# Kernel optimization log

Hardware: AMD Instinct MI355X
Metric: run time of the kernel (lower is better)

Reference implementation:

```python
import jax, jax.numpy as jnp
import numpy as np

D_MODEL = 1024
D = 512
B = 32
L = 1024


def setup_inputs() -> dict:
    key = jax.random.key(0)
    ks = jax.random.split(key, 8)
    s = 1.0 / np.sqrt(D_MODEL)
    x = jax.random.normal(ks[0], (B, L, D_MODEL), dtype=jnp.float32)
    mask = jnp.ones((B, 1, L), dtype=jnp.int32)  # padding mask; 1 = keep
    Wq = jax.random.uniform(ks[1], (D, D_MODEL), jnp.float32, -s, s)
    bq = jax.random.uniform(ks[2], (D,), jnp.float32, -s, s)
    Wk = jax.random.uniform(ks[3], (D, D_MODEL), jnp.float32, -s, s)
    bk = jax.random.uniform(ks[4], (D,), jnp.float32, -s, s)
    Wv = jax.random.uniform(ks[5], (D, D_MODEL), jnp.float32, -s, s)
    bv = jax.random.uniform(ks[6], (D,), jnp.float32, -s, s)
    return {"x": x, "Wq": Wq, "bq": bq, "Wk": Wk, "bk": bk, "Wv": Wv, "bv": bv, "mask": mask}


def reference(x, Wq, bq, Wk, bk, Wv, bv, mask):
    Bq, Lq, _ = x.shape
    q = jnp.einsum('blc,dc->bld', x, Wq) + bq  # [B,L,D]
    k = jnp.einsum('blc,dc->bld', x, Wk) + bk
    v = jnp.einsum('blc,dc->bld', x, Wv) + bv
    scale = k.shape[-1] ** -0.5
    weights = jnp.einsum('bid,bjd->bij', q, k) * scale  # [B,L,L]
    causal = jnp.tril(jnp.ones((Lq, Lq), dtype=bool))
    neg_inf = jnp.float32(-jnp.inf)
    weights = jnp.where(causal[None, :, :], weights, neg_inf)
    weights = jnp.where(mask == 0, neg_inf, weights)  # mask broadcasts [B,1,L]
    weights = jax.nn.softmax(weights, axis=-1)
    # NOTE: source calls self.dropout(weights) but discards result -> no-op
    out = jnp.einsum('bij,bjd->bid', weights, v)
    return jax.nn.relu(out)
```

## Files before the change

### kernel.cpp

```cpp
#include <hip/hip_runtime.h>
#include <hip/hip_bf16.h>
#include <stdint.h>

#define DM 1024
#define DD 512
#define BB 32
#define LL 1024
#define SCALE 0.04419417382415922f
#define MAT ((size_t)BB * LL * DD)

typedef float f32x4 __attribute__((ext_vector_type(4)));
typedef short bf16x8 __attribute__((ext_vector_type(8)));
typedef short bf16x4 __attribute__((ext_vector_type(4)));

__device__ inline unsigned short f2bf(float f) {
    union { float f; uint32_t u; } v; v.f = f;
    uint32_t r = v.u + 0x7fffu + ((v.u >> 16) & 1u);
    return (unsigned short)(r >> 16);
}

__device__ inline bf16x4 cvt4(f32x4 a, float s) {
    bf16x4 r;
    r[0] = (short)f2bf(a[0] * s);
    r[1] = (short)f2bf(a[1] * s);
    r[2] = (short)f2bf(a[2] * s);
    r[3] = (short)f2bf(a[3] * s);
    return r;
}

#define GLOAD_LDS16(gsrc, ldst) \
    __builtin_amdgcn_global_load_lds((const __attribute__((address_space(1))) unsigned int*)(gsrc), \
        (__attribute__((address_space(3))) unsigned int*)(ldst), 16, 0, 0)

__device__ inline void tile_barrier() {
    asm volatile("s_waitcnt vmcnt(0)" ::: "memory");
    __builtin_amdgcn_sched_barrier(0);
    __builtin_amdgcn_s_barrier();
    __builtin_amdgcn_sched_barrier(0);
}

__device__ inline void gate6() {
    asm volatile("s_waitcnt vmcnt(6)" ::: "memory");
    __builtin_amdgcn_sched_barrier(0);
    __builtin_amdgcn_s_barrier();
    __builtin_amdgcn_sched_barrier(0);
}
__device__ inline void gate4() {
    asm volatile("s_waitcnt vmcnt(4)" ::: "memory");
    __builtin_amdgcn_sched_barrier(0);
    __builtin_amdgcn_s_barrier();
    __builtin_amdgcn_sched_barrier(0);
}
__device__ inline void gate2() {
    asm volatile("s_waitcnt vmcnt(2)" ::: "memory");
    __builtin_amdgcn_sched_barrier(0);
    __builtin_amdgcn_s_barrier();
    __builtin_amdgcn_sched_barrier(0);
}
__device__ inline void gate0() {
    asm volatile("s_waitcnt vmcnt(0)" ::: "memory");
    __builtin_amdgcn_sched_barrier(0);
    __builtin_amdgcn_s_barrier();
    __builtin_amdgcn_sched_barrier(0);
}
__device__ inline void gateB() {
    __builtin_amdgcn_sched_barrier(0);
    __builtin_amdgcn_s_barrier();
    __builtin_amdgcn_sched_barrier(0);
}

__global__ __launch_bounds__(256) void cast_x(const float* __restrict__ x,
                                              unsigned short* __restrict__ xb)
{
    size_t idx = (size_t)blockIdx.x * 256 + threadIdx.x;
    size_t base = idx * 8;
    f32x4 a = *(const f32x4*)(x + base);
    f32x4 b = *(const f32x4*)(x + base + 4);
    bf16x4 lo = cvt4(a, 1.0f), hi = cvt4(b, 1.0f);
    bf16x8 o = {lo[0], lo[1], lo[2], lo[3], hi[0], hi[1], hi[2], hi[3]};
    *(bf16x8*)(xb + base) = o;
}

__global__ __launch_bounds__(256) void cast_w(const float* __restrict__ Wq,
                                              const float* __restrict__ Wk,
                                              const float* __restrict__ Wv,
                                              unsigned short* __restrict__ Wb)
{
    size_t idx = (size_t)blockIdx.x * 256 + threadIdx.x;
    int o = (int)(idx >> 16);
    size_t rem = idx & 65535;
    const float* W = (o == 0) ? Wq : (o == 1) ? Wk : Wv;
    float s = (o == 0) ? SCALE : 1.0f;
    size_t base = rem * 8;
    f32x4 a = *(const f32x4*)(W + base);
    f32x4 b = *(const f32x4*)(W + base + 4);
    bf16x4 lo = cvt4(a, s), hi = cvt4(b, s);
    bf16x8 out = {lo[0], lo[1], lo[2], lo[3], hi[0], hi[1], hi[2], hi[3]};
    *(bf16x8*)(Wb + (size_t)o * 524288 + base) = out;
}

__global__ __launch_bounds__(512, 2) void qkv_proj4(
    const unsigned short* __restrict__ xb,
    const unsigned short* __restrict__ Wb,
    const float* __restrict__ bq, const float* __restrict__ bk, const float* __restrict__ bv,
    unsigned short* __restrict__ qkv)
{
    __shared__ __align__(16) unsigned short AL[2][2][8192];
    __shared__ __align__(16) unsigned short BL[2][2][8192];

    const int o = blockIdx.y;
    const float* bias = (o == 0) ? bq : (o == 1) ? bk : bv;
    const float wscale = (o == 0) ? SCALE : 1.0f;
    const unsigned short* W = Wb + (size_t)o * 524288;
    unsigned short* out = qkv + (size_t)o * MAT;

    int wg = blockIdx.x;
    wg = (wg & 7) * 32 + (wg >> 3);
    const int mt = wg >> 1, nt = wg & 1;
    const int rowbase = mt * 256;
    const int colbase = nt * 256;

    const int tid  = threadIdx.x;
    const int lane = tid & 63;
    const int w    = tid >> 6;
    const int wm   = w >> 2;
    const int wn   = w & 3;
    const int l15  = lane & 15, l4 = lane >> 4;
    const int rxor = l15 & 7;

    const int r8   = lane >> 3;
    const int swch = (lane & 7) ^ r8;

    const char* xpanel = (const char*)(xb + (size_t)rowbase * DM);
    const char* wpanel = (const char*)(W  + (size_t)colbase * DM);

    #define STAGE_HALF(panel, T, H, slot) do {                                   \
        _Pragma("unroll")                                                        \
        for (int i2 = 0; i2 < 2; ++i2) {                                         \
            int grp = i2 * 8 + w;                                                \
            GLOAD_LDS16((panel) + ((size_t)((H) * 128 + grp * 8 + r8) * 2048)    \
                            + (size_t)(T) * 128 + swch * 16,                     \
                        (char*)(slot) + grp * 1024);                             \
        }                                                                        \
    } while (0)

    #define RDA(base, mf4, ks) (*(const bf16x8*)((base) + (wm * 64 + (mf4) * 16 + l15) * 128 \
                            + ((((ks) * 4 + l4) ^ rxor) << 4)))
    #define RDB(base, nfl, ks) (*(const bf16x8*)((base) + (wn * 32 + (nfl) * 16 + l15) * 128 \
                            + ((((ks) * 4 + l4) ^ rxor) << 4)))

    f32x4 acc[8][4];
    #pragma unroll
    for (int i = 0; i < 8; ++i)
        #pragma unroll
        for (int j = 0; j < 4; ++j)
            acc[i][j] = (f32x4){0.f, 0.f, 0.f, 0.f};

    bf16x8 aF[4][2], bF[4][2];

    STAGE_HALF(xpanel, 0, 0, &AL[0][0][0]);
    STAGE_HALF(wpanel, 0, 0, &BL[0][0][0]);
    STAGE_HALF(wpanel, 0, 1, &BL[0][1][0]);
    STAGE_HALF(xpanel, 0, 1, &AL[0][1][0]);

    for (int t = 0; t < 16; ++t) {
        const int c = t & 1, cn = c ^ 1;
        const char* A0b = (const char*)&AL[c][0][0];
        const char* A1b = (const char*)&AL[c][1][0];
        const char* B0b = (const char*)&BL[c][0][0];
        const char* B1b = (const char*)&BL[c][1][0];
        const bool st = (t < 15);

        if (st) { STAGE_HALF(xpanel, t + 1, 0, &AL[cn][0][0]); gate6(); } else gate4();
        #pragma unroll
        for (int ks = 0; ks < 2; ++ks) {
            #pragma unroll
            for (int mf = 0; mf < 4; ++mf) aF[mf][ks] = RDA(A0b, mf, ks);
            bF[0][ks] = RDB(B0b, 0, ks);
            bF[1][ks] = RDB(B0b, 1, ks);
        }
        #pragma unroll
        for (int ks = 0; ks < 2; ++ks)
            #pragma unroll
            for (int nf = 0; nf < 2; ++nf)
                #pragma unroll
                for (int mf = 0; mf < 4; ++mf)
                    acc[mf][nf] = __builtin_amdgcn_mfma_f32_16x16x32_bf16(aF[mf][ks], bF[nf][ks], acc[mf][nf], 0, 0, 0);

        if (st) { STAGE_HALF(wpanel, t + 1, 0, &BL[cn][0][0]); gate6(); } else gate2();
        #pragma unroll
        for (int ks = 0; ks < 2; ++ks) {
            bF[2][ks] = RDB(B1b, 0, ks);
            bF[3][ks] = RDB(B1b, 1, ks);
        }
        #pragma unroll
        for (int ks = 0; ks < 2; ++ks)
            #pragma unroll
            for (int nf = 0; nf < 2; ++nf)
                #pragma unroll
                for (int mf = 0; mf < 4; ++mf)
                    acc[mf][2 + nf] = __builtin_amdgcn_mfma_f32_16x16x32_bf16(aF[mf][ks], bF[2 + nf][ks], acc[mf][2 + nf], 0, 0, 0);

        if (st) { STAGE_HALF(wpanel, t + 1, 1, &BL[cn][1][0]); gate6(); } else gate0();
        #pragma unroll
        for (int ks = 0; ks < 2; ++ks)
            #pragma unroll
            for (int mf = 0; mf < 4; ++mf) aF[mf][ks] = RDA(A1b, mf, ks);
        #pragma unroll
        for (int ks = 0; ks < 2; ++ks)
            #pragma unroll
            for (int nf = 0; nf < 2; ++nf)
                #pragma unroll
                for (int mf = 0; mf < 4; ++mf)
                    acc[4 + mf][nf] = __builtin_amdgcn_mfma_f32_16x16x32_bf16(aF[mf][ks], bF[nf][ks], acc[4 + mf][nf], 0, 0, 0);

        if (st) STAGE_HALF(xpanel, t + 1, 1, &AL[cn][1][0]);
        gateB();
        #pragma unroll
        for (int ks = 0; ks < 2; ++ks)
            #pragma unroll
            for (int nf = 0; nf < 2; ++nf)
                #pragma unroll
                for (int mf = 0; mf < 4; ++mf)
                    acc[4 + mf][2 + nf] = __builtin_amdgcn_mfma_f32_16x16x32_bf16(aF[mf][ks], bF[2 + nf][ks], acc[4 + mf][2 + nf], 0, 0, 0);
    }
    #undef STAGE_HALF
    #undef RDA
    #undef RDB

    #pragma unroll
    for (int nf = 0; nf < 4; ++nf) {
        int col = colbase + ((nf < 2) ? wn * 32 + nf * 16 : 128 + wn * 32 + (nf - 2) * 16) + l15;
        float bv_ = bias[col] * wscale;
        #pragma unroll
        for (int mf = 0; mf < 8; ++mf) {
            int row0 = rowbase + ((mf < 4) ? wm * 64 + mf * 16 : 128 + wm * 64 + (mf - 4) * 16) + l4 * 4;
            #pragma unroll
            for (int r = 0; r < 4; ++r)
                out[(size_t)(row0 + r) * DD + col] = f2bf(acc[mf][nf][r] + bv_);
        }
    }
}

__global__ __launch_bounds__(256) void vtrans(const unsigned short* __restrict__ v,
                                              unsigned short* __restrict__ vt)
{
    __shared__ unsigned short T[64][72];
    const int lt = blockIdx.x, dt = blockIdx.y, b = blockIdx.z;
    const int t = threadIdx.x;
    const unsigned short* src = v + ((size_t)(b * LL + lt * 64)) * DD + dt * 64;
    #pragma unroll
    for (int it = 0; it < 2; ++it) {
        int r  = (t >> 3) + it * 32;
        int c0 = (t & 7) * 8;
        bf16x8 x = *(const bf16x8*)(src + (size_t)r * DD + c0);
        *(bf16x4*)&T[r][c0]     = (bf16x4){x[0], x[1], x[2], x[3]};
        *(bf16x4*)&T[r][c0 + 4] = (bf16x4){x[4], x[5], x[6], x[7]};
    }
    __syncthreads();
    unsigned short* dst = vt + ((size_t)(b * DD + dt * 64)) * LL + lt * 64;
    #pragma unroll
    for (int it = 0; it < 2; ++it) {
        int d  = (t >> 3) + it * 32;
        int c0 = (t & 7) * 8;
        bf16x8 o;
        #pragma unroll
        for (int e = 0; e < 8; ++e) o[e] = T[c0 + e][d];
        *(bf16x8*)(dst + (size_t)d * LL + c0) = o;
    }
}

__global__ __launch_bounds__(256, 1) void attn3(
    const unsigned short* __restrict__ qkv,
    const unsigned short* __restrict__ vt,
    const int* __restrict__ mask,
    float* __restrict__ outp)
{
    __shared__ __align__(16) unsigned short KtL[2][16384];
    __shared__ __align__(16) unsigned short VtL[2][16384];
    __shared__ __align__(16) unsigned short Pw[4][16][36];
    __shared__ float mbias[1024];

    const int bx = blockIdx.x;
    const int h = bx >> 8, i = bx & 255;
    const int b = i & 31;
    const int qtx = (i >> 5) & 7;
    const int qt = h ? qtx : 15 - qtx;

    const int tid = threadIdx.x, lane = tid & 63, w = tid >> 6;
    const int l15 = lane & 15, l4 = lane >> 4;
    const int lsw = lane * 16;

    const unsigned short* q = qkv;
    const unsigned short* k = qkv + MAT;
    const char* kb  = (const char*)k + ((size_t)b * LL) * DD * 2;
    const char* vtb = (const char*)vt + ((size_t)b * DD) * LL * 2;

    {
        const int* mp = mask + b * LL;
        #pragma unroll
        for (int j = 0; j < 4; ++j)
            mbias[tid * 4 + j] = mp[tid * 4 + j] ? 0.0f : -1e30f;
    }

    bf16x8 qf[16];
    {
        const unsigned short* qp = q + ((size_t)(b * LL + qt * 64 + w * 16 + l15)) * DD + l4 * 8;
        #pragma unroll
        for (int ks = 0; ks < 16; ++ks)
            qf[ks] = *(const bf16x8*)(qp + ks * 32);
    }

    f32x4 oacc[32];
    #pragma unroll
    for (int n = 0; n < 32; ++n) oacc[n] = (f32x4){0.f, 0.f, 0.f, 0.f};
    float mrow[4] = {-1e30f, -1e30f, -1e30f, -1e30f};
    float lrow[4] = {0.f, 0.f, 0.f, 0.f};

    const int jtmax = 2 * qt + 1;

    #define STAGE_KV(JT, BUF) do {                                              \
        const char* kt = kb + ((size_t)(JT) << 15);                             \
        char* ldsK = (char*)&KtL[(BUF)][0];                                     \
        _Pragma("unroll")                                                       \
        for (int i2 = 0; i2 < 8; ++i2) {                                        \
            int row = i2 * 4 + w;                                               \
            GLOAD_LDS16(kt + (row << 10) + (lsw ^ ((row & 7) << 4)),            \
                        ldsK + (row << 10));                                    \
        }                                                                       \
        const char* vtj = vtb + ((size_t)(JT) << 6);                            \
        char* ldsV = (char*)&VtL[(BUF)][0];                                     \
        _Pragma("unroll")                                                       \
        for (int i2 = 0; i2 < 8; ++i2) {                                        \
            int c0 = i2 * 256 + w * 64;                                         \
            int c  = c0 + lane;                                                 \
            GLOAD_LDS16(vtj + ((size_t)(c >> 2) << 11) + ((c & 3) << 4),        \
                        ldsV + c0 * 16);                                        \
        }                                                                       \
    } while (0)

    STAGE_KV(0, 0);
    __syncthreads();

    const int swz = (l15 & 7) << 4;

    for (int jt = 0; jt <= jtmax; ++jt) {
        const int cur = jt & 1;
        if (jt < jtmax) STAGE_KV(jt + 1, cur ^ 1);

        const char* Kc = (const char*)&KtL[cur][0];
        f32x4 sacc[2];
        sacc[0] = (f32x4){0.f, 0.f, 0.f, 0.f};
        sacc[1] = (f32x4){0.f, 0.f, 0.f, 0.f};
        #pragma unroll
        for (int ks = 0; ks < 16; ++ks) {
            int coloff = ((ks << 6) + (l4 << 4)) ^ swz;
            #pragma unroll
            for (int nf = 0; nf < 2; ++nf) {
                const bf16x8 kf = *(const bf16x8*)(Kc + ((nf * 16 + l15) << 10) + coloff);
                sacc[nf] = __builtin_amdgcn_mfma_f32_16x16x32_bf16(qf[ks], kf, sacc[nf], 0, 0, 0);
            }
        }

        const bool diag = (jt >= 2 * qt);
        float s[2][4];
        #pragma unroll
        for (int nf = 0; nf < 2; ++nf) {
            float bb_ = mbias[jt * 32 + nf * 16 + l15];
            #pragma unroll
            for (int r = 0; r < 4; ++r) {
                float val = sacc[nf][r] + bb_;
                if (diag) {
                    int gi = qt * 64 + w * 16 + l4 * 4 + r;
                    int gj = jt * 32 + nf * 16 + l15;
                    val = (gj <= gi) ? val : -3e38f;
                }
                s[nf][r] = val;
            }
        }
        float pm[4];
        #pragma unroll
        for (int r = 0; r < 4; ++r) {
            float mx = fmaxf(s[0][r], s[1][r]);
            mx = fmaxf(mx, __shfl_xor(mx, 1));
            mx = fmaxf(mx, __shfl_xor(mx, 2));
            mx = fmaxf(mx, __shfl_xor(mx, 4));
            mx = fmaxf(mx, __shfl_xor(mx, 8));
            pm[r] = mx;
        }
        bool need = false;
        #pragma unroll
        for (int r = 0; r < 4; ++r) need |= (pm[r] - mrow[r] > 8.0f);
        if (__any(need)) {
            #pragma unroll
            for (int r = 0; r < 4; ++r) {
                float mn = fmaxf(mrow[r], pm[r]);
                float corr = __expf(mrow[r] - mn);
                mrow[r] = mn;
                lrow[r] *= corr;
                #pragma unroll
                for (int n = 0; n < 32; ++n) oacc[n][r] *= corr;
            }
        }
        #pragma unroll
        for (int r = 0; r < 4; ++r) {
            float ls = 0.f;
            #pragma unroll
            for (int nf = 0; nf < 2; ++nf) {
                float p = __expf(s[nf][r] - mrow[r]);
                ls += p;
                Pw[w][l4 * 4 + r][nf * 16 + l15] = f2bf(p);
            }
            ls += __shfl_xor(ls, 1);
            ls += __shfl_xor(ls, 2);
            ls += __shfl_xor(ls, 4);
            ls += __shfl_xor(ls, 8);
            lrow[r] += ls;
        }

        const bf16x8 pa = *(const bf16x8*)&Pw[w][l15][l4 * 8];
        const char* Vc = (const char*)&VtL[cur][0];
        #pragma unroll
        for (int n = 0; n < 32; ++n) {
            const bf16x8 vb_ = *(const bf16x8*)(Vc + ((n * 16 + l15) << 6) + (l4 << 4));
            oacc[n] = __builtin_amdgcn_mfma_f32_16x16x32_bf16(pa, vb_, oacc[n], 0, 0, 0);
        }

        if (jt < jtmax) tile_barrier();
    }

    float inv[4];
    #pragma unroll
    for (int r = 0; r < 4; ++r) inv[r] = 1.0f / lrow[r];
    float* op = outp + ((size_t)(b * LL + qt * 64 + w * 16 + l4 * 4)) * DD + l15;
    #pragma unroll
    for (int n = 0; n < 32; ++n)
        #pragma unroll
        for (int r = 0; r < 4; ++r)
            op[(size_t)r * DD + n * 16] = fmaxf(oacc[n][r] * inv[r], 0.f);
    #undef STAGE_KV
}

extern "C" void kernel_launch(void* const* d_in, const int* in_sizes, int n_in,
                              void* d_out, int out_size, void* d_ws, size_t ws_size,
                              hipStream_t stream) {
    const float* x  = (const float*)d_in[0];
    const float* Wq = (const float*)d_in[1];
    const float* bq = (const float*)d_in[2];
    const float* Wk = (const float*)d_in[3];
    const float* bk = (const float*)d_in[4];
    const float* Wv = (const float*)d_in[5];
    const float* bv = (const float*)d_in[6];
    const int* mask = (const int*)d_in[7];

    unsigned short* qkv = (unsigned short*)d_ws;
    unsigned short* v   = qkv + 2 * MAT;
    unsigned short* vtp = qkv + 3 * MAT;
    unsigned short* Wb  = vtp;
    unsigned short* xb  = (unsigned short*)d_out;
    float* out = (float*)d_out;

    cast_x<<<16384, 256, 0, stream>>>(x, xb);
    cast_w<<<768, 256, 0, stream>>>(Wq, Wk, Wv, Wb);
    qkv_proj4<<<dim3(256, 3), 512, 0, stream>>>(xb, Wb, bq, bk, bv, qkv);
    vtrans<<<dim3(16, 8, 32), 256, 0, stream>>>(v, vtp);
    attn3<<<dim3(512), 256, 0, stream>>>(qkv, vtp, mask, out);
}
```

Before: 278.6 us.

## Single-buffer K/V LDS tiles with split staging and read mask from global

```diff
diff --git a/kernel.cpp b/kernel.cpp
--- a/kernel.cpp
+++ b/kernel.cpp
@@ -32,7 +32,7 @@
     __builtin_amdgcn_global_load_lds((const __attribute__((address_space(1))) unsigned int*)(gsrc), \
         (__attribute__((address_space(3))) unsigned int*)(ldst), 16, 0, 0)
 
-__device__ inline void tile_barrier() {
+__device__ inline void publish_barrier() {
     asm volatile("s_waitcnt vmcnt(0)" ::: "memory");
     __builtin_amdgcn_sched_barrier(0);
     __builtin_amdgcn_s_barrier();
@@ -64,6 +64,12 @@
     __builtin_amdgcn_sched_barrier(0);
 }
 __device__ inline void gateB() {
+    __builtin_amdgcn_sched_barrier(0);
+    __builtin_amdgcn_s_barrier();
+    __builtin_amdgcn_sched_barrier(0);
+}
+__device__ inline void gate8() {
+    asm volatile("s_waitcnt vmcnt(8)" ::: "memory");
     __builtin_amdgcn_sched_barrier(0);
     __builtin_amdgcn_s_barrier();
     __builtin_amdgcn_sched_barrier(0);
@@ -270,22 +276,19 @@
     }
 }
 
-__global__ __launch_bounds__(256, 1) void attn3(
+__global__ __launch_bounds__(256) void attn6(
     const unsigned short* __restrict__ qkv,
     const unsigned short* __restrict__ vt,
     const int* __restrict__ mask,
     float* __restrict__ outp)
 {
-    __shared__ __align__(16) unsigned short KtL[2][16384];
-    __shared__ __align__(16) unsigned short VtL[2][16384];
+    __shared__ __align__(16) unsigned short KtL[16384];
+    __shared__ __align__(16) unsigned short VtL[16384];
     __shared__ __align__(16) unsigned short Pw[4][16][36];
-    __shared__ float mbias[1024];
 
     const int bx = blockIdx.x;
-    const int h = bx >> 8, i = bx & 255;
-    const int b = i & 31;
-    const int qtx = (i >> 5) & 7;
-    const int qt = h ? qtx : 15 - qtx;
+    const int qt = (bx >> 4) & 15;
+    const int b  = (bx & 15) | ((bx >> 8) << 4);
 
     const int tid = threadIdx.x, lane = tid & 63, w = tid >> 6;
     const int l15 = lane & 15, l4 = lane >> 4;
@@ -295,13 +298,7 @@
     const unsigned short* k = qkv + MAT;
     const char* kb  = (const char*)k + ((size_t)b * LL) * DD * 2;
     const char* vtb = (const char*)vt + ((size_t)b * DD) * LL * 2;
-
-    {
-        const int* mp = mask + b * LL;
-        #pragma unroll
-        for (int j = 0; j < 4; ++j)
-            mbias[tid * 4 + j] = mp[tid * 4 + j] ? 0.0f : -1e30f;
-    }
+    const int* mp = mask + b * LL;
 
     bf16x8 qf[16];
     {
@@ -319,36 +316,35 @@
 
     const int jtmax = 2 * qt + 1;
 
-    #define STAGE_KV(JT, BUF) do {                                              \
+    #define STAGE_K6(JT) do {                                                   \
         const char* kt = kb + ((size_t)(JT) << 15);                             \
-        char* ldsK = (char*)&KtL[(BUF)][0];                                     \
         _Pragma("unroll")                                                       \
         for (int i2 = 0; i2 < 8; ++i2) {                                        \
             int row = i2 * 4 + w;                                               \
             GLOAD_LDS16(kt + (row << 10) + (lsw ^ ((row & 7) << 4)),            \
-                        ldsK + (row << 10));                                    \
+                        (char*)KtL + (row << 10));                              \
         }                                                                       \
+    } while (0)
+
+    #define STAGE_V6(JT) do {                                                   \
         const char* vtj = vtb + ((size_t)(JT) << 6);                            \
-        char* ldsV = (char*)&VtL[(BUF)][0];                                     \
         _Pragma("unroll")                                                       \
         for (int i2 = 0; i2 < 8; ++i2) {                                        \
             int c0 = i2 * 256 + w * 64;                                         \
             int c  = c0 + lane;                                                 \
             GLOAD_LDS16(vtj + ((size_t)(c >> 2) << 11) + ((c & 3) << 4),        \
-                        ldsV + c0 * 16);                                        \
+                        (char*)VtL + c0 * 16);                                  \
         }                                                                       \
     } while (0)
 
-    STAGE_KV(0, 0);
-    __syncthreads();
+    STAGE_K6(0);
+    STAGE_V6(0);
 
     const int swz = (l15 & 7) << 4;
 
     for (int jt = 0; jt <= jtmax; ++jt) {
-        const int cur = jt & 1;
-        if (jt < jtmax) STAGE_KV(jt + 1, cur ^ 1);
-
-        const char* Kc = (const char*)&KtL[cur][0];
+        gate8();
+
         f32x4 sacc[2];
         sacc[0] = (f32x4){0.f, 0.f, 0.f, 0.f};
         sacc[1] = (f32x4){0.f, 0.f, 0.f, 0.f};
@@ -357,16 +353,23 @@
             int coloff = ((ks << 6) + (l4 << 4)) ^ swz;
             #pragma unroll
             for (int nf = 0; nf < 2; ++nf) {
-                const bf16x8 kf = *(const bf16x8*)(Kc + ((nf * 16 + l15) << 10) + coloff);
+                const bf16x8 kf = *(const bf16x8*)((const char*)KtL + ((nf * 16 + l15) << 10) + coloff);
                 sacc[nf] = __builtin_amdgcn_mfma_f32_16x16x32_bf16(qf[ks], kf, sacc[nf], 0, 0, 0);
             }
         }
 
+        __builtin_amdgcn_sched_barrier(0);
+        __syncthreads();
+        __builtin_amdgcn_sched_barrier(0);
+        if (jt < jtmax) STAGE_K6(jt + 1);
+
         const bool diag = (jt >= 2 * qt);
+        float mb0 = mp[jt * 32 + l15]      ? 0.0f : -1e30f;
+        float mb1 = mp[jt * 32 + 16 + l15] ? 0.0f : -1e30f;
         float s[2][4];
         #pragma unroll
         for (int nf = 0; nf < 2; ++nf) {
-            float bb_ = mbias[jt * 32 + nf * 16 + l15];
+            float bb_ = nf ? mb1 : mb0;
             #pragma unroll
             for (int r = 0; r < 4; ++r) {
                 float val = sacc[nf][r] + bb_;
@@ -419,14 +422,16 @@
         }
 
         const bf16x8 pa = *(const bf16x8*)&Pw[w][l15][l4 * 8];
-        const char* Vc = (const char*)&VtL[cur][0];
         #pragma unroll
         for (int n = 0; n < 32; ++n) {
-            const bf16x8 vb_ = *(const bf16x8*)(Vc + ((n * 16 + l15) << 6) + (l4 << 4));
+            const bf16x8 vb_ = *(const bf16x8*)((const char*)VtL + ((n * 16 + l15) << 6) + (l4 << 4));
             oacc[n] = __builtin_amdgcn_mfma_f32_16x16x32_bf16(pa, vb_, oacc[n], 0, 0, 0);
         }
 
-        if (jt < jtmax) tile_barrier();
+        if (jt < jtmax) {
+            gateB();
+            STAGE_V6(jt + 1);
+        }
     }
 
     float inv[4];
@@ -438,7 +443,8 @@
         #pragma unroll
         for (int r = 0; r < 4; ++r)
             op[(size_t)r * DD + n * 16] = fmaxf(oacc[n][r] * inv[r], 0.f);
-    #undef STAGE_KV
+    #undef STAGE_K6
+    #undef STAGE_V6
 }
 
 extern "C" void kernel_launch(void* const* d_in, const int* in_sizes, int n_in,
@@ -464,5 +470,5 @@
     cast_w<<<768, 256, 0, stream>>>(Wq, Wk, Wv, Wb);
     qkv_proj4<<<dim3(256, 3), 512, 0, stream>>>(xb, Wb, bq, bk, bv, qkv);
     vtrans<<<dim3(16, 8, 32), 256, 0, stream>>>(v, vtp);
-    attn3<<<dim3(512), 256, 0, stream>>>(qkv, vtp, mask, out);
-}
+    attn6<<<dim3(512), 256, 0, stream>>>(qkv, vtp, mask, out);
+}
```

Result: slower. 335.9 us (+20.6%).

## Split fused flash attention into QK GEMM, row softmax and PV GEMM kernels

Applied to the files above, without the earlier changes.

```diff
diff --git a/kernel.cpp b/kernel.cpp
--- a/kernel.cpp
+++ b/kernel.cpp
@@ -17,6 +17,10 @@
     union { float f; uint32_t u; } v; v.f = f;
     uint32_t r = v.u + 0x7fffu + ((v.u >> 16) & 1u);
     return (unsigned short)(r >> 16);
+}
+__device__ inline float bf2f(unsigned short u) {
+    union { uint32_t u; float f; } v; v.u = ((uint32_t)u) << 16;
+    return v.f;
 }
 
 __device__ inline bf16x4 cvt4(f32x4 a, float s) {
@@ -32,13 +36,12 @@
     __builtin_amdgcn_global_load_lds((const __attribute__((address_space(1))) unsigned int*)(gsrc), \
         (__attribute__((address_space(3))) unsigned int*)(ldst), 16, 0, 0)
 
-__device__ inline void tile_barrier() {
+__device__ inline void publish_barrier() {
     asm volatile("s_waitcnt vmcnt(0)" ::: "memory");
     __builtin_amdgcn_sched_barrier(0);
     __builtin_amdgcn_s_barrier();
     __builtin_amdgcn_sched_barrier(0);
 }
-
 __device__ inline void gate6() {
     asm volatile("s_waitcnt vmcnt(6)" ::: "memory");
     __builtin_amdgcn_sched_barrier(0);
@@ -270,31 +273,105 @@
     }
 }
 
-__global__ __launch_bounds__(256, 1) void attn3(
+__global__ __launch_bounds__(256, 2) void sgemm_qk(
     const unsigned short* __restrict__ qkv,
-    const unsigned short* __restrict__ vt,
-    const int* __restrict__ mask,
-    float* __restrict__ outp)
-{
-    __shared__ __align__(16) unsigned short KtL[2][16384];
-    __shared__ __align__(16) unsigned short VtL[2][16384];
-    __shared__ __align__(16) unsigned short Pw[4][16][36];
-    __shared__ float mbias[1024];
-
-    const int bx = blockIdx.x;
-    const int h = bx >> 8, i = bx & 255;
-    const int b = i & 31;
-    const int qtx = (i >> 5) & 7;
-    const int qt = h ? qtx : 15 - qtx;
-
-    const int tid = threadIdx.x, lane = tid & 63, w = tid >> 6;
-    const int l15 = lane & 15, l4 = lane >> 4;
-    const int lsw = lane * 16;
+    unsigned short* __restrict__ S)
+{
+    __shared__ __align__(16) unsigned short At[2][8192];
+    __shared__ __align__(16) unsigned short Bt[2][8192];
+
+    int wg = blockIdx.x;
+    wg = (wg & 7) * 144 + (wg >> 3);
+    const int b = wg / 36;
+    const int t36 = wg % 36;
+    int mt = 0, accq = 0;
+    while (accq + mt + 1 <= t36) { ++mt; accq += mt; }
+    const int nt = t36 - accq;
+
+    const int tid  = threadIdx.x;
+    const int lane = tid & 63;
+    const int w    = tid >> 6;
+    const int wr   = (w >> 1) * 64;
+    const int wc   = (w & 1) * 64;
+    const int l15  = lane & 15, l4 = lane >> 4;
+
+    const int r8   = lane >> 3;
+    const int swch = (lane & 7) ^ r8;
 
     const unsigned short* q = qkv;
     const unsigned short* k = qkv + MAT;
-    const char* kb  = (const char*)k + ((size_t)b * LL) * DD * 2;
-    const char* vtb = (const char*)vt + ((size_t)b * DD) * LL * 2;
+    const char* apanel = (const char*)(q + ((size_t)(b * LL) + mt * 128) * DD);
+    const char* bpanel = (const char*)(k + ((size_t)(b * LL) + nt * 128) * DD);
+
+    f32x4 acc[4][4];
+    #pragma unroll
+    for (int i = 0; i < 4; ++i)
+        #pragma unroll
+        for (int j = 0; j < 4; ++j)
+            acc[i][j] = (f32x4){0.f, 0.f, 0.f, 0.f};
+
+    #define STAGE_QK(KK, BUF) do {                                               \
+        _Pragma("unroll")                                                        \
+        for (int i2 = 0; i2 < 4; ++i2) {                                         \
+            int grp = i2 * 4 + w;                                                \
+            size_t rowoff = (size_t)(grp * 8 + r8) * 1024 + (KK) * 2 + swch * 16;\
+            GLOAD_LDS16(apanel + rowoff, (char*)&At[BUF][0] + grp * 1024);       \
+            GLOAD_LDS16(bpanel + rowoff, (char*)&Bt[BUF][0] + grp * 1024);       \
+        }                                                                        \
+    } while (0)
+
+    STAGE_QK(0, 0);
+    __syncthreads();
+
+    for (int t = 0; t < 8; ++t) {
+        const int cur = t & 1;
+        if (t < 7) STAGE_QK((t + 1) * 64, cur ^ 1);
+
+        const char* Ab = (const char*)&At[cur][0];
+        const char* Bb = (const char*)&Bt[cur][0];
+        #pragma unroll
+        for (int ks = 0; ks < 2; ++ks) {
+            bf16x8 af[4], bf_[4];
+            const int ch = (ks * 4 + l4) ^ (l15 & 7);
+            #pragma unroll
+            for (int m = 0; m < 4; ++m)
+                af[m] = *(const bf16x8*)(Ab + (wr + m * 16 + l15) * 128 + (ch << 4));
+            #pragma unroll
+            for (int n = 0; n < 4; ++n)
+                bf_[n] = *(const bf16x8*)(Bb + (wc + n * 16 + l15) * 128 + (ch << 4));
+            #pragma unroll
+            for (int n = 0; n < 4; ++n)
+                #pragma unroll
+                for (int m = 0; m < 4; ++m)
+                    acc[m][n] = __builtin_amdgcn_mfma_f32_16x16x32_bf16(af[m], bf_[n], acc[m][n], 0, 0, 0);
+        }
+
+        if (t < 7) publish_barrier();
+    }
+    #undef STAGE_QK
+
+    unsigned short* sp = S + ((size_t)(b * LL) + mt * 128) * LL + nt * 128;
+    #pragma unroll
+    for (int n = 0; n < 4; ++n) {
+        int col = wc + n * 16 + l15;
+        #pragma unroll
+        for (int m = 0; m < 4; ++m) {
+            int row0 = wr + m * 16 + l4 * 4;
+            #pragma unroll
+            for (int r = 0; r < 4; ++r)
+                sp[(size_t)(row0 + r) * LL + col] = f2bf(acc[m][n][r]);
+        }
+    }
+}
+
+__global__ __launch_bounds__(256) void softmax_rows(
+    const unsigned short* __restrict__ S,
+    const int* __restrict__ mask,
+    unsigned short* __restrict__ P)
+{
+    __shared__ float mbias[1024];
+    const int rc = blockIdx.x, b = blockIdx.y;
+    const int tid = threadIdx.x, lane = tid & 63, w = tid >> 6;
 
     {
         const int* mp = mask + b * LL;
@@ -302,143 +379,146 @@
         for (int j = 0; j < 4; ++j)
             mbias[tid * 4 + j] = mp[tid * 4 + j] ? 0.0f : -1e30f;
     }
-
-    bf16x8 qf[16];
-    {
-        const unsigned short* qp = q + ((size_t)(b * LL + qt * 64 + w * 16 + l15)) * DD + l4 * 8;
-        #pragma unroll
-        for (int ks = 0; ks < 16; ++ks)
-            qf[ks] = *(const bf16x8*)(qp + ks * 32);
-    }
-
-    f32x4 oacc[32];
-    #pragma unroll
-    for (int n = 0; n < 32; ++n) oacc[n] = (f32x4){0.f, 0.f, 0.f, 0.f};
-    float mrow[4] = {-1e30f, -1e30f, -1e30f, -1e30f};
-    float lrow[4] = {0.f, 0.f, 0.f, 0.f};
-
-    const int jtmax = 2 * qt + 1;
-
-    #define STAGE_KV(JT, BUF) do {                                              \
-        const char* kt = kb + ((size_t)(JT) << 15);                             \
-        char* ldsK = (char*)&KtL[(BUF)][0];                                     \
-        _Pragma("unroll")                                                       \
-        for (int i2 = 0; i2 < 8; ++i2) {                                        \
-            int row = i2 * 4 + w;                                               \
-            GLOAD_LDS16(kt + (row << 10) + (lsw ^ ((row & 7) << 4)),            \
-                        ldsK + (row << 10));                                    \
-        }                                                                       \
-        const char* vtj = vtb + ((size_t)(JT) << 6);                            \
-        char* ldsV = (char*)&VtL[(BUF)][0];                                     \
-        _Pragma("unroll")                                                       \
-        for (int i2 = 0; i2 < 8; ++i2) {                                        \
-            int c0 = i2 * 256 + w * 64;                                         \
-            int c  = c0 + lane;                                                 \
-            GLOAD_LDS16(vtj + ((size_t)(c >> 2) << 11) + ((c & 3) << 4),        \
-                        ldsV + c0 * 16);                                        \
-        }                                                                       \
+    __syncthreads();
+
+    const int j0 = lane * 16;
+    for (int i = 0; i < 32; ++i) {
+        const int r = rc * 128 + i * 4 + w;
+        const unsigned short* srow = S + ((size_t)(b * LL) + r) * LL;
+
+        bf16x8 v0 = {0,0,0,0,0,0,0,0}, v1 = {0,0,0,0,0,0,0,0};
+        if (j0 <= r)     v0 = *(const bf16x8*)(srow + j0);
+        if (j0 + 8 <= r) v1 = *(const bf16x8*)(srow + j0 + 8);
+
+        float s[16];
+        #pragma unroll
+        for (int e = 0; e < 8; ++e) {
+            int j = j0 + e;
+            s[e]     = (j <= r)     ? bf2f((unsigned short)v0[e]) + mbias[j]     : -3e38f;
+            s[8 + e] = (j + 8 <= r) ? bf2f((unsigned short)v1[e]) + mbias[j + 8] : -3e38f;
+        }
+        float mx = s[0];
+        #pragma unroll
+        for (int e = 1; e < 16; ++e) mx = fmaxf(mx, s[e]);
+        mx = fmaxf(mx, __shfl_xor(mx, 1));
+        mx = fmaxf(mx, __shfl_xor(mx, 2));
+        mx = fmaxf(mx, __shfl_xor(mx, 4));
+        mx = fmaxf(mx, __shfl_xor(mx, 8));
+        mx = fmaxf(mx, __shfl_xor(mx, 16));
+        mx = fmaxf(mx, __shfl_xor(mx, 32));
+
+        float p[16], ls = 0.f;
+        #pragma unroll
+        for (int e = 0; e < 16; ++e) { p[e] = __expf(s[e] - mx); ls += p[e]; }
+        ls += __shfl_xor(ls, 1);
+        ls += __shfl_xor(ls, 2);
+        ls += __shfl_xor(ls, 4);
+        ls += __shfl_xor(ls, 8);
+        ls += __shfl_xor(ls, 16);
+        ls += __shfl_xor(ls, 32);
+        const float inv = 1.0f / ls;
+
+        bf16x8 o0, o1;
+        #pragma unroll
+        for (int e = 0; e < 8; ++e) {
+            o0[e] = (short)f2bf(p[e] * inv);
+            o1[e] = (short)f2bf(p[8 + e] * inv);
+        }
+        unsigned short* prow = P + ((size_t)(b * LL) + r) * LL;
+        *(bf16x8*)(prow + j0)     = o0;
+        *(bf16x8*)(prow + j0 + 8) = o1;
+    }
+}
+
+__global__ __launch_bounds__(256, 2) void pv_gemm(
+    const unsigned short* __restrict__ P,
+    const unsigned short* __restrict__ vt,
+    float* __restrict__ outp)
+{
+    __shared__ __align__(16) unsigned short At[2][8192];
+    __shared__ __align__(16) unsigned short Bt[2][8192];
+
+    int wg = blockIdx.x;
+    wg = (wg & 7) * 128 + (wg >> 3);
+    const int b  = wg >> 5;
+    const int rr = wg & 31;
+    const int rt = 7 - (rr >> 2);
+    const int ct = rr & 3;
+
+    const int tid  = threadIdx.x;
+    const int lane = tid & 63;
+    const int w    = tid >> 6;
+    const int wr   = (w >> 1) * 64;
+    const int wc   = (w & 1) * 64;
+    const int l15  = lane & 15, l4 = lane >> 4;
+
+    const int r8   = lane >> 3;
+    const int swch = (lane & 7) ^ r8;
+
+    const char* apanel = (const char*)(P  + ((size_t)(b * LL) + rt * 128) * LL);
+    const char* bpanel = (const char*)(vt + ((size_t)(b * DD) + ct * 128) * LL);
+
+    const int NT = (rt + 1) * 2;
+
+    f32x4 acc[4][4];
+    #pragma unroll
+    for (int i = 0; i < 4; ++i)
+        #pragma unroll
+        for (int j = 0; j < 4; ++j)
+            acc[i][j] = (f32x4){0.f, 0.f, 0.f, 0.f};
+
+    #define STAGE_PV(KK, BUF) do {                                               \
+        _Pragma("unroll")                                                        \
+        for (int i2 = 0; i2 < 4; ++i2) {                                         \
+            int grp = i2 * 4 + w;                                                \
+            size_t rowoff = (size_t)(grp * 8 + r8) * 2048 + (KK) * 2 + swch * 16;\
+            GLOAD_LDS16(apanel + rowoff, (char*)&At[BUF][0] + grp * 1024);       \
+            GLOAD_LDS16(bpanel + rowoff, (char*)&Bt[BUF][0] + grp * 1024);       \
+        }                                                                        \
     } while (0)
 
-    STAGE_KV(0, 0);
+    STAGE_PV(0, 0);
     __syncthreads();
 
-    const int swz = (l15 & 7) << 4;
-
-    for (int jt = 0; jt <= jtmax; ++jt) {
-        const int cur = jt & 1;
-        if (jt < jtmax) STAGE_KV(jt + 1, cur ^ 1);
-
-        const char* Kc = (const char*)&KtL[cur][0];
-        f32x4 sacc[2];
-        sacc[0] = (f32x4){0.f, 0.f, 0.f, 0.f};
-        sacc[1] = (f32x4){0.f, 0.f, 0.f, 0.f};
-        #pragma unroll
-        for (int ks = 0; ks < 16; ++ks) {
-            int coloff = ((ks << 6) + (l4 << 4)) ^ swz;
-            #pragma unroll
-            for (int nf = 0; nf < 2; ++nf) {
-                const bf16x8 kf = *(const bf16x8*)(Kc + ((nf * 16 + l15) << 10) + coloff);
-                sacc[nf] = __builtin_amdgcn_mfma_f32_16x16x32_bf16(qf[ks], kf, sacc[nf], 0, 0, 0);
-            }
-        }
-
-        const bool diag = (jt >= 2 * qt);
-        float s[2][4];
-        #pragma unroll
-        for (int nf = 0; nf < 2; ++nf) {
-            float bb_ = mbias[jt * 32 + nf * 16 + l15];
-            #pragma unroll
-            for (int r = 0; r < 4; ++r) {
-                float val = sacc[nf][r] + bb_;
-                if (diag) {
-                    int gi = qt * 64 + w * 16 + l4 * 4 + r;
-                    int gj = jt * 32 + nf * 16 + l15;
-                    val = (gj <= gi) ? val : -3e38f;
-                }
-                s[nf][r] = val;
-            }
-        }
-        float pm[4];
-        #pragma unroll
-        for (int r = 0; r < 4; ++r) {
-            float mx = fmaxf(s[0][r], s[1][r]);
-            mx = fmaxf(mx, __shfl_xor(mx, 1));
-            mx = fmaxf(mx, __shfl_xor(mx, 2));
-            mx = fmaxf(mx, __shfl_xor(mx, 4));
-            mx = fmaxf(mx, __shfl_xor(mx, 8));
-            pm[r] = mx;
-        }
-        bool need = false;
-        #pragma unroll
-        for (int r = 0; r < 4; ++r) need |= (pm[r] - mrow[r] > 8.0f);
-        if (__any(need)) {
-            #pragma unroll
-            for (int r = 0; r < 4; ++r) {
-                float mn = fmaxf(mrow[r], pm[r]);
-                float corr = __expf(mrow[r] - mn);
-                mrow[r] = mn;
-                lrow[r] *= corr;
+    for (int t = 0; t < NT; ++t) {
+        const int cur = t & 1;
+        if (t < NT - 1) STAGE_PV((t + 1) * 64, cur ^ 1);
+
+        const char* Ab = (const char*)&At[cur][0];
+        const char* Bb = (const char*)&Bt[cur][0];
+        #pragma unroll
+        for (int ks = 0; ks < 2; ++ks) {
+            bf16x8 af[4], bf_[4];
+            const int ch = (ks * 4 + l4) ^ (l15 & 7);
+            #pragma unroll
+            for (int m = 0; m < 4; ++m)
+                af[m] = *(const bf16x8*)(Ab + (wr + m * 16 + l15) * 128 + (ch << 4));
+            #pragma unroll
+            for (int n = 0; n < 4; ++n)
+                bf_[n] = *(const bf16x8*)(Bb + (wc + n * 16 + l15) * 128 + (ch << 4));
+            #pragma unroll
+            for (int n = 0; n < 4; ++n)
                 #pragma unroll
-                for (int n = 0; n < 32; ++n) oacc[n][r] *= corr;
-            }
-        }
-        #pragma unroll
-        for (int r = 0; r < 4; ++r) {
-            float ls = 0.f;
-            #pragma unroll
-            for (int nf = 0; nf < 2; ++nf) {
-                float p = __expf(s[nf][r] - mrow[r]);
-                ls += p;
-                Pw[w][l4 * 4 + r][nf * 16 + l15] = f2bf(p);
-            }
-            ls += __shfl_xor(ls, 1);
-            ls += __shfl_xor(ls, 2);
-            ls += __shfl_xor(ls, 4);
-            ls += __shfl_xor(ls, 8);
-            lrow[r] += ls;
-        }
-
-        const bf16x8 pa = *(const bf16x8*)&Pw[w][l15][l4 * 8];
-        const char* Vc = (const char*)&VtL[cur][0];
-        #pragma unroll
-        for (int n = 0; n < 32; ++n) {
-            const bf16x8 vb_ = *(const bf16x8*)(Vc + ((n * 16 + l15) << 6) + (l4 << 4));
-            oacc[n] = __builtin_amdgcn_mfma_f32_16x16x32_bf16(pa, vb_, oacc[n], 0, 0, 0);
-        }
-
-        if (jt < jtmax) tile_barrier();
-    }
-
-    float inv[4];
-    #pragma unroll
-    for (int r = 0; r < 4; ++r) inv[r] = 1.0f / lrow[r];
-    float* op = outp + ((size_t)(b * LL + qt * 64 + w * 16 + l4 * 4)) * DD + l15;
-    #pragma unroll
-    for (int n = 0; n < 32; ++n)
-        #pragma unroll
-        for (int r = 0; r < 4; ++r)
-            op[(size_t)r * DD + n * 16] = fmaxf(oacc[n][r] * inv[r], 0.f);
-    #undef STAGE_KV
+                for (int m = 0; m < 4; ++m)
+                    acc[m][n] = __builtin_amdgcn_mfma_f32_16x16x32_bf16(af[m], bf_[n], acc[m][n], 0, 0, 0);
+        }
+
+        if (t < NT - 1) publish_barrier();
+    }
+    #undef STAGE_PV
+
+    float* op = outp + ((size_t)(b * LL) + rt * 128) * DD + ct * 128;
+    #pragma unroll
+    for (int n = 0; n < 4; ++n) {
+        int col = wc + n * 16 + l15;
+        #pragma unroll
+        for (int m = 0; m < 4; ++m) {
+            int row0 = wr + m * 16 + l4 * 4;
+            #pragma unroll
+            for (int r = 0; r < 4; ++r)
+                op[(size_t)(row0 + r) * DD + col] = fmaxf(acc[m][n][r], 0.f);
+        }
+    }
 }
 
 extern "C" void kernel_launch(void* const* d_in, const int* in_sizes, int n_in,
@@ -458,11 +538,15 @@
     unsigned short* vtp = qkv + 3 * MAT;
     unsigned short* Wb  = vtp;
     unsigned short* xb  = (unsigned short*)d_out;
+    unsigned short* S   = (unsigned short*)d_out;
+    unsigned short* Pp  = qkv;
     float* out = (float*)d_out;
 
     cast_x<<<16384, 256, 0, stream>>>(x, xb);
     cast_w<<<768, 256, 0, stream>>>(Wq, Wk, Wv, Wb);
     qkv_proj4<<<dim3(256, 3), 512, 0, stream>>>(xb, Wb, bq, bk, bv, qkv);
     vtrans<<<dim3(16, 8, 32), 256, 0, stream>>>(v, vtp);
-    attn3<<<dim3(512), 256, 0, stream>>>(qkv, vtp, mask, out);
-}
+    sgemm_qk<<<dim3(1152), 256, 0, stream>>>(qkv, S);
+    softmax_rows<<<dim3(8, 32), 256, 0, stream>>>(S, mask, Pp);
+    pv_gemm<<<dim3(1024), 256, 0, stream>>>(Pp, vtp, out);
+}
```

Result: no change. 277.5 us (-0.4%).
